# Kernel optimization log

Measured on AMD Instinct MI355X. Metric: run time of the kernel, lower is better.

## Reference

```python
import jax, jax.numpy as jnp
import numpy as np

RETRIEVAL_TEMP = 0.5
TOP_K = 50


def setup_inputs() -> dict:
    key = jax.random.key(0)
    ks = jax.random.split(key, 8)
    B, N, D = 64, 50000, 2048
    return {
        "query_vec": jax.random.normal(ks[0], (B, D), dtype=jnp.float32),
        "vritti_types": jax.random.randint(ks[1], (N,), 0, 5, dtype=jnp.int64),
        "seed_memory": jax.random.normal(ks[2], (N, D), dtype=jnp.float32) * 0.02,
        "karma_scores": jax.random.normal(ks[3], (N,), dtype=jnp.float32) * 0.1,
        "vritti_bias": jnp.array([0.15, 0.1, -0.05, 0.0, -1.0], dtype=jnp.float32),
        "W1": jax.random.normal(ks[4], (D, 2 * D), dtype=jnp.float32) * (1.0 / np.sqrt(D)),
        "b1": jnp.zeros((2 * D,), dtype=jnp.float32),
        "W2": jax.random.normal(ks[5], (2 * D, D), dtype=jnp.float32) * (1.0 / np.sqrt(2 * D)),
        "b2": jnp.zeros((D,), dtype=jnp.float32),
    }


def reference(query_vec, vritti_types, seed_memory, karma_scores, vritti_bias, W1, b1, W2, b2):
    # Query MLP: Linear -> GELU (exact, erf-based, torch default) -> Linear
    h = jax.nn.gelu(query_vec @ W1 + b1, approximate=False)      # [B, 2D]
    q = h @ W2 + b2                                              # [B, D]
    # Similarity against the full seed bank
    sims = jnp.einsum("bd,nd->bn", q, seed_memory)               # [B, N]
    # Karma gating (elementwise, broadcast over batch)
    karma_gate = jax.nn.sigmoid((karma_scores + 0.3) * 10.0)     # [N]
    sims = sims * karma_gate[None, :]
    # Per-seed vritti bias (gather from 5-entry table)
    sims = sims + vritti_bias[vritti_types][None, :]
    # Temperature softmax over all seeds
    attention_weights = jax.nn.softmax(sims / RETRIEVAL_TEMP, axis=-1)  # [B, N]
    # Top-k retrieval (sorted descending, matches torch.topk)
    topk_values, topk_indices = jax.lax.top_k(attention_weights, TOP_K)  # [B, K]
    # Vectorized per-batch gather of retrieved seed embeddings
    chitta_field = seed_memory[topk_indices]                     # [B, K, D]
    return (chitta_field, attention_weights, topk_indices)
```

## Files before the change

kernel.cpp:

```cpp
#include <hip/hip_runtime.h>
#include <math.h>

#define B 64
#define D 2048
#define H 4096
#define NSEED 50000
#define KTOP 50
#define NCAND 64
#define CEMIT 20
#define NCHUNKS 64
#define CHUNK_SZ 782

#define WS_LOGITS   0
#define WS_H        3200000
#define WS_Q2       (WS_H + B*H)
#define WS_PART     (WS_Q2 + B*D)
#define WS_CVAL     (WS_PART + 1048576)
#define WS_CIDX     (WS_CVAL + 262144)
#define WS_CM       (WS_CIDX + 262144)
#define WS_CS       (WS_CM + 4096)
#define WS_RM       (WS_CS + 4096)
#define WS_RS       (WS_RM + 64)
#define WS_Q2HL     (WS_RS + 64)
#define WSP_CAND    200000
#define WSP_RVAL    220000
#define WSP_TIDX    240000

typedef short s16x8 __attribute__((ext_vector_type(8)));
typedef float f32x4 __attribute__((ext_vector_type(4)));

__device__ __forceinline__ unsigned short bf16_rne(float x)
{
    unsigned int b = __float_as_uint(x);
    b += 0x7FFFu + ((b >> 16) & 1u);
    return (unsigned short)(b >> 16);
}
__device__ __forceinline__ float bf16_tof(unsigned short h)
{
    return __uint_as_float(((unsigned int)h) << 16);
}

__global__ __launch_bounds__(256) void gemm64_kernel(
    const float* __restrict__ A, const float* __restrict__ W,
    float* __restrict__ part, int K, int N, int kcK, int nBlocks)
{
    __shared__ float As[32][68];
    __shared__ float Bs[32][68];

    const int tid = threadIdx.x;
    const int nb = blockIdx.x % nBlocks;
    const int kc = blockIdx.x / nBlocks;
    const int kbeg = kc * kcK;

    const int tidm = tid >> 5;
    const int tidn = tid & 31;
    const int m0 = tidm * 8;
    const int n0g = nb * 64 + tidn * 2;

    float acc[8][2];
#pragma unroll
    for (int i = 0; i < 8; ++i) { acc[i][0] = 0.f; acc[i][1] = 0.f; }

    for (int k0 = kbeg; k0 < kbeg + kcK; k0 += 32) {
        __syncthreads();
#pragma unroll
        for (int i = 0; i < 2; ++i) {
            int q = tid + i * 256;
            int row = q >> 3, c = q & 7;
            float4 va = *(const float4*)(A + (size_t)row * K + k0 + c * 4);
            As[c * 4 + 0][row] = va.x; As[c * 4 + 1][row] = va.y;
            As[c * 4 + 2][row] = va.z; As[c * 4 + 3][row] = va.w;
            int wr = q >> 4, wc = q & 15;
            float4 vb = *(const float4*)(W + (size_t)(k0 + wr) * N + nb * 64 + wc * 4);
            *(float4*)&Bs[wr][wc * 4] = vb;
        }
        __syncthreads();
#pragma unroll
        for (int kk = 0; kk < 32; ++kk) {
            float4 a0 = *(const float4*)&As[kk][m0];
            float4 a1 = *(const float4*)&As[kk][m0 + 4];
            float2 b = *(const float2*)&Bs[kk][tidn * 2];
            float av[8] = {a0.x, a0.y, a0.z, a0.w, a1.x, a1.y, a1.z, a1.w};
#pragma unroll
            for (int i = 0; i < 8; ++i) {
                acc[i][0] += av[i] * b.x;
                acc[i][1] += av[i] * b.y;
            }
        }
    }
#pragma unroll
    for (int i = 0; i < 8; ++i) {
        float2 v; v.x = acc[i][0]; v.y = acc[i][1];
        *(float2*)(part + (size_t)(kc * B + m0 + i) * N + n0g) = v;
    }
}

__global__ void mlp_reduce_kernel(const float* __restrict__ part,
                                  const float* __restrict__ bias,
                                  float* __restrict__ out, int N, int nchunks, int gelu,
                                  unsigned short* __restrict__ uh,
                                  unsigned short* __restrict__ ul)
{
    int e = blockIdx.x * 256 + threadIdx.x;
    int b = e / N, j = e - b * N;
    float s = bias[j];
    for (int c = 0; c < nchunks; ++c)
        s += part[(size_t)(c * B + b) * N + j];
    if (gelu)
        s = 0.5f * s * (1.0f + erff(s * 0.70710678118654752f));
    out[e] = s;
    if (uh) {
        unsigned short h = bf16_rne(s);
        uh[e] = h;
        ul[e] = bf16_rne(s - bf16_tof(h));
    }
}

__device__ __forceinline__ bool types_is_i64(const int* t)
{
    int acc = 0;
#pragma unroll
    for (int j = 0; j < 16; ++j) acc |= t[2 * j + 1];
    return acc == 0;
}

__global__ __launch_bounds__(256) void sims_mfma_kernel(
    const unsigned short* __restrict__ q2h, const unsigned short* __restrict__ q2l,
    const float* __restrict__ seed,
    const float* __restrict__ karma, const int* __restrict__ types,
    const float* __restrict__ vbias, float* __restrict__ logits)
{
    __shared__ __align__(16) unsigned short Ash[2][64][72];
    __shared__ __align__(16) unsigned short Asl[2][64][72];

    const int tid = threadIdx.x;
    const int n0 = blockIdx.x * 64;
    const int lane = tid & 63;
    const int wv  = tid >> 6;
    const int l15 = lane & 15;
    const int lg  = lane >> 4;

    const int srow = tid >> 2;
    const int seg  = tid & 3;

    const int nrow = n0 + wv * 16 + l15;
    const bool nvalid = nrow < NSEED;
    const float* brow = seed + (size_t)nrow * D + 8 * lg;
    const size_t aoff = (size_t)srow * D + 16 * seg;

    f32x4 acc[4];
#pragma unroll
    for (int t = 0; t < 4; ++t) acc[t] = (f32x4){0.f, 0.f, 0.f, 0.f};

    s16x8 a0ha, a0hb, a0la, a0lb;
    s16x8 a1ha, a1hb, a1la, a1lb;
    float4 b00, b01, b02, b03;
    float4 b10, b11, b12, b13;

    a0ha = *(const s16x8*)(q2h + aoff);
    a0hb = *(const s16x8*)(q2h + aoff + 8);
    a0la = *(const s16x8*)(q2l + aoff);
    a0lb = *(const s16x8*)(q2l + aoff + 8);
    a1ha = *(const s16x8*)(q2h + aoff + 64);
    a1hb = *(const s16x8*)(q2h + aoff + 72);
    a1la = *(const s16x8*)(q2l + aoff + 64);
    a1lb = *(const s16x8*)(q2l + aoff + 72);
    b00 = b01 = b02 = b03 = make_float4(0.f, 0.f, 0.f, 0.f);
    b10 = b11 = b12 = b13 = make_float4(0.f, 0.f, 0.f, 0.f);
    if (nvalid) {
        b00 = *(const float4*)(brow);      b01 = *(const float4*)(brow + 4);
        b02 = *(const float4*)(brow + 32); b03 = *(const float4*)(brow + 36);
        b10 = *(const float4*)(brow + 64); b11 = *(const float4*)(brow + 68);
        b12 = *(const float4*)(brow + 96); b13 = *(const float4*)(brow + 100);
    }

#define SIMS_CONV(F0, F1, BH, BL)                                          \
    {                                                                      \
        float xs[8] = {F0.x, F0.y, F0.z, F0.w, F1.x, F1.y, F1.z, F1.w};    \
        _Pragma("unroll")                                                  \
        for (int j = 0; j < 8; ++j) {                                      \
            unsigned short hu = bf16_rne(xs[j]);                           \
            BH[j] = (short)hu;                                             \
            BL[j] = (short)bf16_rne(xs[j] - bf16_tof(hu));                 \
        }                                                                  \
    }

#define SIMS_MFMA(BUF, KS, BH, BL)                                         \
    _Pragma("unroll")                                                      \
    for (int t = 0; t < 4; ++t) {                                          \
        s16x8 ah = *(const s16x8*)&Ash[BUF][t * 16 + l15][KS * 32 + 8 * lg]; \
        s16x8 al = *(const s16x8*)&Asl[BUF][t * 16 + l15][KS * 32 + 8 * lg]; \
        acc[t] = __builtin_amdgcn_mfma_f32_16x16x32_bf16(ah, BH, acc[t], 0, 0, 0); \
        acc[t] = __builtin_amdgcn_mfma_f32_16x16x32_bf16(al, BH, acc[t], 0, 0, 0); \
        acc[t] = __builtin_amdgcn_mfma_f32_16x16x32_bf16(ah, BL, acc[t], 0, 0, 0); \
    }

    for (int u = 0; u < 16; ++u) {
        *(s16x8*)&Ash[0][srow][16 * seg]     = a0ha;
        *(s16x8*)&Ash[0][srow][16 * seg + 8] = a0hb;
        *(s16x8*)&Asl[0][srow][16 * seg]     = a0la;
        *(s16x8*)&Asl[0][srow][16 * seg + 8] = a0lb;
        float4 n0a = make_float4(0.f, 0.f, 0.f, 0.f), n0b = n0a, n0c = n0a, n0d = n0a;
        if (u < 15) {
            const int kb = 128 * u + 128;
            a0ha = *(const s16x8*)(q2h + aoff + kb);
            a0hb = *(const s16x8*)(q2h + aoff + kb + 8);
            a0la = *(const s16x8*)(q2l + aoff + kb);
            a0lb = *(const s16x8*)(q2l + aoff + kb + 8);
            if (nvalid) {
                n0a = *(const float4*)(brow + kb);      n0b = *(const float4*)(brow + kb + 4);
                n0c = *(const float4*)(brow + kb + 32); n0d = *(const float4*)(brow + kb + 36);
            }
        }
        __syncthreads();
        {
            s16x8 bh, bl;
            SIMS_CONV(b00, b01, bh, bl);
            SIMS_MFMA(0, 0, bh, bl);
            SIMS_CONV(b02, b03, bh, bl);
            SIMS_MFMA(0, 1, bh, bl);
        }
        b00 = n0a; b01 = n0b; b02 = n0c; b03 = n0d;

        *(s16x8*)&Ash[1][srow][16 * seg]     = a1ha;
        *(s16x8*)&Ash[1][srow][16 * seg + 8] = a1hb;
        *(s16x8*)&Asl[1][srow][16 * seg]     = a1la;
        *(s16x8*)&Asl[1][srow][16 * seg + 8] = a1lb;
        float4 n1a = make_float4(0.f, 0.f, 0.f, 0.f), n1b = n1a, n1c = n1a, n1d = n1a;
        if (u < 15) {
            const int kb = 128 * u + 192;
            a1ha = *(const s16x8*)(q2h + aoff + kb);
            a1hb = *(const s16x8*)(q2h + aoff + kb + 8);
            a1la = *(const s16x8*)(q2l + aoff + kb);
            a1lb = *(const s16x8*)(q2l + aoff + kb + 8);
            if (nvalid) {
                n1a = *(const float4*)(brow + kb);      n1b = *(const float4*)(brow + kb + 4);
                n1c = *(const float4*)(brow + kb + 32); n1d = *(const float4*)(brow + kb + 36);
            }
        }
        __syncthreads();
        {
            s16x8 bh, bl;
            SIMS_CONV(b10, b11, bh, bl);
            SIMS_MFMA(1, 0, bh, bl);
            SIMS_CONV(b12, b13, bh, bl);
            SIMS_MFMA(1, 1, bh, bl);
        }
        b10 = n1a; b11 = n1b; b12 = n1c; b13 = n1d;
    }
#undef SIMS_CONV
#undef SIMS_MFMA

    if (nvalid) {
        const bool i64 = types_is_i64(types);
        float ka = karma[nrow];
        float gate = 1.0f / (1.0f + expf(-(ka + 0.3f) * 10.0f));
        int ty = i64 ? types[2 * nrow] : types[nrow];
        float bias = vbias[ty];
#pragma unroll
        for (int t = 0; t < 4; ++t) {
#pragma unroll
            for (int r = 0; r < 4; ++r) {
                int m = t * 16 + lg * 4 + r;
                logits[(size_t)m * NSEED + nrow] = acc[t][r] * gate + bias;
            }
        }
    }
}

__global__ __launch_bounds__(64) void chunk_topk_kernel(
    const float* __restrict__ logits,
    float* __restrict__ chunk_m, float* __restrict__ chunk_s,
    float* __restrict__ cand_val, int* __restrict__ cand_idx)
{
    const int bid = blockIdx.x;
    const int row = bid >> 6, chunk = bid & 63;
    const int start = chunk * CHUNK_SZ;
    const int end = min(start + CHUNK_SZ, NSEED);
    const int lane = threadIdx.x;
    const float* Lrow = logits + (size_t)row * NSEED;

    float v[13];
#pragma unroll
    for (int j = 0; j < 13; ++j) {
        int e = start + lane + j * 64;
        v[j] = (e < end) ? Lrow[e] : -INFINITY;
    }

    float m = v[0];
#pragma unroll
    for (int j = 1; j < 13; ++j) m = fmaxf(m, v[j]);
    float s = 0.f;
#pragma unroll
    for (int j = 0; j < 13; ++j) s += expf(2.f * (v[j] - m));
#pragma unroll
    for (int d = 1; d < 64; d <<= 1) {
        float mo = __shfl_xor(m, d);
        float so = __shfl_xor(s, d);
        float nm = fmaxf(m, mo);
        s = s * expf(2.f * (m - nm)) + so * expf(2.f * (mo - nm));
        m = nm;
    }
    if (lane == 0) { chunk_m[bid] = m; chunk_s[bid] = s; }

    for (int it = 0; it < CEMIT; ++it) {
        float bv = v[0]; int bj = 0;
#pragma unroll
        for (int j = 1; j < 13; ++j)
            if (v[j] > bv) { bv = v[j]; bj = j; }
        int bi = start + lane + bj * 64;
#pragma unroll
        for (int d = 1; d < 64; d <<= 1) {
            float ov = __shfl_xor(bv, d);
            int oi = __shfl_xor(bi, d);
            if (ov > bv || (ov == bv && oi < bi)) { bv = ov; bi = oi; }
        }
        if (lane == 0) {
            cand_val[bid * CEMIT + it] = bv;
            cand_idx[bid * CEMIT + it] = bi;
        }
#pragma unroll
        for (int j = 0; j < 13; ++j)
            if (start + lane + j * 64 == bi) v[j] = -INFINITY;
    }
}

__global__ __launch_bounds__(256) void merge_topk_kernel(
    const float* __restrict__ chunk_m, const float* __restrict__ chunk_s,
    const float* __restrict__ cand_val, const int* __restrict__ cand_idx,
    float* __restrict__ row_M, float* __restrict__ row_rS,
    int* __restrict__ cand2)
{
    const int row = blockIdx.x;
    const int tid = threadIdx.x;
    const int lane = tid & 63, wave = tid >> 6;
    __shared__ float rv[4];
    __shared__ int ri[4];

    if (wave == 0) {
        float m = chunk_m[row * 64 + lane];
        float s = chunk_s[row * 64 + lane];
#pragma unroll
        for (int d = 1; d < 64; d <<= 1) {
            float mo = __shfl_xor(m, d);
            float so = __shfl_xor(s, d);
            float nm = fmaxf(m, mo);
            s = s * expf(2.f * (m - nm)) + so * expf(2.f * (mo - nm));
            m = nm;
        }
        if (lane == 0) { row_M[row] = m; row_rS[row] = 1.0f / s; }
    }

    float v[5]; int ix[5];
#pragma unroll
    for (int j = 0; j < 5; ++j) {
        int e = tid + j * 256;
        v[j] = cand_val[row * (NCHUNKS * CEMIT) + e];
        ix[j] = cand_idx[row * (NCHUNKS * CEMIT) + e];
    }

    for (int it = 0; it < NCAND; ++it) {
        float bv = v[0]; int bi = ix[0];
#pragma unroll
        for (int j = 1; j < 5; ++j)
            if (v[j] > bv || (v[j] == bv && ix[j] < bi)) { bv = v[j]; bi = ix[j]; }
#pragma unroll
        for (int d = 1; d < 64; d <<= 1) {
            float ov = __shfl_xor(bv, d);
            int oi = __shfl_xor(bi, d);
            if (ov > bv || (ov == bv && oi < bi)) { bv = ov; bi = oi; }
        }
        if (lane == 0) { rv[wave] = bv; ri[wave] = bi; }
        __syncthreads();
        float wv = rv[0]; int wi = ri[0];
#pragma unroll
        for (int w = 1; w < 4; ++w)
            if (rv[w] > wv || (rv[w] == wv && ri[w] < wi)) { wv = rv[w]; wi = ri[w]; }
        __syncthreads();
        if (tid == 0) cand2[row * NCAND + it] = wi;
#pragma unroll
        for (int j = 0; j < 5; ++j)
            if (ix[j] == wi) v[j] = -INFINITY;
    }
}

__global__ __launch_bounds__(256) void rescore_kernel(
    const float* __restrict__ q2, const float* __restrict__ seed,
    const float* __restrict__ karma, const int* __restrict__ types,
    const float* __restrict__ vbias, const int* __restrict__ cand2,
    float* __restrict__ rvals)
{
    const int row = blockIdx.y;
    const int wv = threadIdx.x >> 6, lane = threadIdx.x & 63;
    const int ci = blockIdx.x * 4 + wv;
    const int idx = cand2[row * NCAND + ci];
    const float* qrow = q2 + (size_t)row * D;
    const float* srow = seed + (size_t)idx * D;

    double s = 0.0;
#pragma unroll
    for (int i = 0; i < 8; ++i) {
        float4 a = *(const float4*)(qrow + lane * 4 + i * 256);
        float4 b = *(const float4*)(srow + lane * 4 + i * 256);
        s += (double)a.x * (double)b.x + (double)a.y * (double)b.y
           + (double)a.z * (double)b.z + (double)a.w * (double)b.w;
    }
#pragma unroll
    for (int d = 1; d < 64; d <<= 1) s += __shfl_xor(s, d);

    if (lane == 0) {
        float ka = karma[idx];
        float gate = 1.0f / (1.0f + expf(-(ka + 0.3f) * 10.0f));
        bool i64 = types_is_i64(types);
        int ty = i64 ? types[2 * idx] : types[idx];
        rvals[row * NCAND + ci] = (float)s * gate + vbias[ty];
    }
}

__global__ __launch_bounds__(64) void final50_kernel(
    const float* __restrict__ rvals, const int* __restrict__ cand2,
    float* __restrict__ out_idx_f, int* __restrict__ topk_idx)
{
    const int row = blockIdx.x;
    const int lane = threadIdx.x;

    float v = rvals[row * NCAND + lane];
    int ix = cand2[row * NCAND + lane];

    for (int it = 0; it < KTOP; ++it) {
        float bv = v; int bi = ix;
#pragma unroll
        for (int d = 1; d < 64; d <<= 1) {
            float ov = __shfl_xor(bv, d);
            int oi = __shfl_xor(bi, d);
            if (ov > bv || (ov == bv && oi < bi)) { bv = ov; bi = oi; }
        }
        if (lane == 0) {
            out_idx_f[row * KTOP + it] = (float)bi;
            topk_idx[row * KTOP + it] = bi;
        }
        if (ix == bi) v = -INFINITY;
    }
}

__global__ void weights_kernel(const float* __restrict__ logits,
                               const float* __restrict__ row_M,
                               const float* __restrict__ row_rS,
                               float* __restrict__ attn)
{
    const int row = blockIdx.y;
    const int f = blockIdx.x * 256 + threadIdx.x;
    if (f >= NSEED / 4) return;
    const float M = row_M[row], rS = row_rS[row];
    float4 l = ((const float4*)(logits + (size_t)row * NSEED))[f];
    float4 w;
    w.x = expf(2.f * (l.x - M)) * rS;
    w.y = expf(2.f * (l.y - M)) * rS;
    w.z = expf(2.f * (l.z - M)) * rS;
    w.w = expf(2.f * (l.w - M)) * rS;
    ((float4*)(attn + (size_t)row * NSEED))[f] = w;
}

__global__ void gather_kernel(const float* __restrict__ seed,
                              const int* __restrict__ topk_idx,
                              float* __restrict__ chitta)
{
    const int k = blockIdx.x, row = blockIdx.y;
    const int idx = topk_idx[row * KTOP + k];
    const float4* src = (const float4*)(seed + (size_t)idx * D);
    float4* dst = (float4*)(chitta + (size_t)(row * KTOP + k) * D);
#pragma unroll
    for (int j = 0; j < 2; ++j)
        dst[threadIdx.x + j * 256] = src[threadIdx.x + j * 256];
}

extern "C" void kernel_launch(void* const* d_in, const int* in_sizes, int n_in,
                              void* d_out, int out_size, void* d_ws, size_t ws_size,
                              hipStream_t stream)
{
    const float* query = (const float*)d_in[0];
    const int*   types = (const int*)d_in[1];
    const float* seed  = (const float*)d_in[2];
    const float* karma = (const float*)d_in[3];
    const float* vbias = (const float*)d_in[4];
    const float* W1    = (const float*)d_in[5];
    const float* b1    = (const float*)d_in[6];
    const float* W2    = (const float*)d_in[7];
    const float* b2    = (const float*)d_in[8];

    float* ws = (float*)d_ws;
    float* logits = ws + WS_LOGITS;
    float* h      = ws + WS_H;
    float* q2     = ws + WS_Q2;
    float* part   = ws + WS_PART;
    float* cval   = ws + WS_CVAL;
    int*   cidx   = (int*)(ws + WS_CIDX);
    float* cm     = ws + WS_CM;
    float* cs     = ws + WS_CS;
    float* rM     = ws + WS_RM;
    float* rS     = ws + WS_RS;

    unsigned short* q2h = (unsigned short*)(ws + WS_Q2HL);
    unsigned short* q2l = q2h + (size_t)B * D;

    int*   cand2 = (int*)(part + WSP_CAND);
    float* rvals = part + WSP_RVAL;
    int*   tidx  = (int*)(part + WSP_TIDX);

    float* outv   = (float*)d_out;
    float* chitta = outv;
    float* attn   = outv + (size_t)B * KTOP * D;
    float* oidxf  = attn + (size_t)B * NSEED;

    gemm64_kernel<<<256, 256, 0, stream>>>(query, W1, part, D, H, 512, H / 64);
    mlp_reduce_kernel<<<(B * H) / 256, 256, 0, stream>>>(part, b1, h, H, 4, 1, nullptr, nullptr);
    gemm64_kernel<<<256, 256, 0, stream>>>(h, W2, part, H, D, 512, D / 64);
    mlp_reduce_kernel<<<(B * D) / 256, 256, 0, stream>>>(part, b2, q2, D, 8, 0, q2h, q2l);
    sims_mfma_kernel<<<(NSEED + 63) / 64, 256, 0, stream>>>(q2h, q2l, seed, karma, types, vbias, logits);
    chunk_topk_kernel<<<B * NCHUNKS, 64, 0, stream>>>(logits, cm, cs, cval, cidx);
    merge_topk_kernel<<<B, 256, 0, stream>>>(cm, cs, cval, cidx, rM, rS, cand2);
    rescore_kernel<<<dim3(NCAND / 4, B), 256, 0, stream>>>(q2, seed, karma, types, vbias, cand2, rvals);
    final50_kernel<<<B, 64, 0, stream>>>(rvals, cand2, oidxf, tidx);
    weights_kernel<<<dim3((NSEED / 4 + 255) / 256, B), 256, 0, stream>>>(logits, rM, rS, attn);
    gather_kernel<<<dim3(KTOP, B), 256, 0, stream>>>(seed, tidx, chitta);
}
```

Measured before the change: 339.9 us.

## Double-buffer MLP GEMM tiles with register prefetch and 4x4 thread tiles

Rewrites the FP32 MLP GEMM to prefetch the next K-slice into registers while computing on a double-buffered shared-memory tile, which drops one barrier per step. Each thread now computes a 4x4 micro-tile instead of 8x2, a squarer shape meant to reduce shared-memory loads per FMA. The first GEMM doubles its K-split to 8 chunks of 256, launching more blocks for occupancy at the cost of more partial sums to reduce. Partial sums are written into the logits workspace region instead of the separate part buffer, relying on logits being overwritten later.

```diff
diff --git a/kernel.cpp b/kernel.cpp
--- a/kernel.cpp
+++ b/kernel.cpp
@@ -40,58 +40,82 @@
     return __uint_as_float(((unsigned int)h) << 16);
 }
 
-__global__ __launch_bounds__(256) void gemm64_kernel(
+__global__ __launch_bounds__(256) void gemm64p_kernel(
     const float* __restrict__ A, const float* __restrict__ W,
     float* __restrict__ part, int K, int N, int kcK, int nBlocks)
 {
-    __shared__ float As[32][68];
-    __shared__ float Bs[32][68];
+    __shared__ float As[2][32][68];
+    __shared__ float Bs[2][32][68];
 
     const int tid = threadIdx.x;
     const int nb = blockIdx.x % nBlocks;
     const int kc = blockIdx.x / nBlocks;
     const int kbeg = kc * kcK;
 
-    const int tidm = tid >> 5;
-    const int tidn = tid & 31;
-    const int m0 = tidm * 8;
-    const int n0g = nb * 64 + tidn * 2;
-
-    float acc[8][2];
-#pragma unroll
-    for (int i = 0; i < 8; ++i) { acc[i][0] = 0.f; acc[i][1] = 0.f; }
-
-    for (int k0 = kbeg; k0 < kbeg + kcK; k0 += 32) {
+    const int tidm = tid >> 4;
+    const int tidn = tid & 15;
+    const int m0 = tidm * 4;
+    const int n0 = tidn * 4;
+
+    const int ar0 = tid >> 3, ac0 = tid & 7;
+    const int wr0 = tid >> 4, wc0 = tid & 15;
+
+    const float* Aptr0 = A + (size_t)ar0 * K + kbeg + ac0 * 4;
+    const float* Aptr1 = A + (size_t)(ar0 + 32) * K + kbeg + ac0 * 4;
+    const float* Wptr0 = W + (size_t)(kbeg + wr0) * N + nb * 64 + wc0 * 4;
+    const float* Wptr1 = W + (size_t)(kbeg + wr0 + 16) * N + nb * 64 + wc0 * 4;
+
+    float acc[4][4];
+#pragma unroll
+    for (int i = 0; i < 4; ++i)
+#pragma unroll
+        for (int j = 0; j < 4; ++j) acc[i][j] = 0.f;
+
+    float4 pa0 = *(const float4*)(Aptr0);
+    float4 pa1 = *(const float4*)(Aptr1);
+    float4 pb0 = *(const float4*)(Wptr0);
+    float4 pb1 = *(const float4*)(Wptr1);
+
+    const int nsteps = kcK / 32;
+    for (int s = 0; s < nsteps; ++s) {
+        const int buf = s & 1;
+        As[buf][ac0 * 4 + 0][ar0] = pa0.x;
+        As[buf][ac0 * 4 + 1][ar0] = pa0.y;
+        As[buf][ac0 * 4 + 2][ar0] = pa0.z;
+        As[buf][ac0 * 4 + 3][ar0] = pa0.w;
+        As[buf][ac0 * 4 + 0][ar0 + 32] = pa1.x;
+        As[buf][ac0 * 4 + 1][ar0 + 32] = pa1.y;
+        As[buf][ac0 * 4 + 2][ar0 + 32] = pa1.z;
+        As[buf][ac0 * 4 + 3][ar0 + 32] = pa1.w;
+        *(float4*)&Bs[buf][wr0][wc0 * 4] = pb0;
+        *(float4*)&Bs[buf][wr0 + 16][wc0 * 4] = pb1;
+        if (s + 1 < nsteps) {
+            const int ko = 32 * (s + 1);
+            pa0 = *(const float4*)(Aptr0 + ko);
+            pa1 = *(const float4*)(Aptr1 + ko);
+            pb0 = *(const float4*)(Wptr0 + (size_t)ko * N);
+            pb1 = *(const float4*)(Wptr1 + (size_t)ko * N);
+        }
         __syncthreads();
 #pragma unroll
-        for (int i = 0; i < 2; ++i) {
-            int q = tid + i * 256;
-            int row = q >> 3, c = q & 7;
-            float4 va = *(const float4*)(A + (size_t)row * K + k0 + c * 4);
-            As[c * 4 + 0][row] = va.x; As[c * 4 + 1][row] = va.y;
-            As[c * 4 + 2][row] = va.z; As[c * 4 + 3][row] = va.w;
-            int wr = q >> 4, wc = q & 15;
-            float4 vb = *(const float4*)(W + (size_t)(k0 + wr) * N + nb * 64 + wc * 4);
-            *(float4*)&Bs[wr][wc * 4] = vb;
-        }
-        __syncthreads();
-#pragma unroll
         for (int kk = 0; kk < 32; ++kk) {
-            float4 a0 = *(const float4*)&As[kk][m0];
-            float4 a1 = *(const float4*)&As[kk][m0 + 4];
-            float2 b = *(const float2*)&Bs[kk][tidn * 2];
-            float av[8] = {a0.x, a0.y, a0.z, a0.w, a1.x, a1.y, a1.z, a1.w};
-#pragma unroll
-            for (int i = 0; i < 8; ++i) {
-                acc[i][0] += av[i] * b.x;
-                acc[i][1] += av[i] * b.y;
-            }
-        }
-    }
-#pragma unroll
-    for (int i = 0; i < 8; ++i) {
-        float2 v; v.x = acc[i][0]; v.y = acc[i][1];
-        *(float2*)(part + (size_t)(kc * B + m0 + i) * N + n0g) = v;
+            float4 a = *(const float4*)&As[buf][kk][m0];
+            float4 b = *(const float4*)&Bs[buf][kk][n0];
+            float av[4] = {a.x, a.y, a.z, a.w};
+            float bv[4] = {b.x, b.y, b.z, b.w};
+#pragma unroll
+            for (int i = 0; i < 4; ++i)
+#pragma unroll
+                for (int j = 0; j < 4; ++j)
+                    acc[i][j] += av[i] * bv[j];
+        }
+    }
+
+#pragma unroll
+    for (int i = 0; i < 4; ++i) {
+        float4 v;
+        v.x = acc[i][0]; v.y = acc[i][1]; v.z = acc[i][2]; v.w = acc[i][3];
+        *(float4*)(part + (size_t)(kc * B + m0 + i) * N + nb * 64 + n0) = v;
     }
 }
 
@@ -512,10 +536,10 @@
     float* attn   = outv + (size_t)B * KTOP * D;
     float* oidxf  = attn + (size_t)B * NSEED;
 
-    gemm64_kernel<<<256, 256, 0, stream>>>(query, W1, part, D, H, 512, H / 64);
-    mlp_reduce_kernel<<<(B * H) / 256, 256, 0, stream>>>(part, b1, h, H, 4, 1, nullptr, nullptr);
-    gemm64_kernel<<<256, 256, 0, stream>>>(h, W2, part, H, D, 512, D / 64);
-    mlp_reduce_kernel<<<(B * D) / 256, 256, 0, stream>>>(part, b2, q2, D, 8, 0, q2h, q2l);
+    gemm64p_kernel<<<64 * 8, 256, 0, stream>>>(query, W1, logits, D, H, 256, 64);
+    mlp_reduce_kernel<<<(B * H) / 256, 256, 0, stream>>>(logits, b1, h, H, 8, 1, nullptr, nullptr);
+    gemm64p_kernel<<<32 * 8, 256, 0, stream>>>(h, W2, logits, H, D, 512, 32);
+    mlp_reduce_kernel<<<(B * D) / 256, 256, 0, stream>>>(logits, b2, q2, D, 8, 0, q2h, q2l);
     sims_mfma_kernel<<<(NSEED + 63) / 64, 256, 0, stream>>>(q2h, q2l, seed, karma, types, vbias, logits);
     chunk_topk_kernel<<<B * NCHUNKS, 64, 0, stream>>>(logits, cm, cs, cval, cidx);
     merge_topk_kernel<<<B, 256, 0, stream>>>(cm, cs, cval, cidx, rM, rS, cand2);
```

Result: faster. 316.3 us (-6.9%).
